# Performance work log

Measured on AMD Instinct MI355X. Metric: run time of the kernel, lower is better.

The kernel has to match this reference:

```python
import jax, jax.numpy as jnp
import numpy as np

D_MODEL = 1024
N_HEAD = 16
HEAD_DIM = D_MODEL // N_HEAD  # 64


def setup_inputs() -> dict:
    key = jax.random.key(0)
    ks = jax.random.split(key, 8)
    B, T, C = 4, 2048, D_MODEL
    s = 0.02
    return {
        "q": jax.random.normal(ks[0], (B, T, C), jnp.float32),
        "k": jax.random.normal(ks[1], (B, T, C), jnp.float32),
        "v": jax.random.normal(ks[2], (B, T, C), jnp.float32),
        "Wq": jax.random.normal(ks[3], (C, C), jnp.float32) * s,
        "Wk": jax.random.normal(ks[4], (C, HEAD_DIM), jnp.float32) * s,
        "Wv": jax.random.normal(ks[5], (C, HEAD_DIM), jnp.float32) * s,
        "Wp": jax.random.normal(ks[6], (C, C), jnp.float32) * s,
        "bp": jnp.zeros((C,), jnp.float32),
    }


def reference(q, k, v, Wq, Wk, Wv, Wp, bp):
    B, T, C = q.shape
    scale = 1.0 / jnp.sqrt(jnp.asarray(HEAD_DIM, q.dtype))
    # projections (torch Linear: x @ W.T, here weights stored as [in, out])
    q_proj = (q @ Wq).reshape(B, T, N_HEAD, HEAD_DIM)  # [B,T,H,D]
    k_proj = k @ Wk  # [B,T,D] single shared KV head
    v_proj = v @ Wv  # [B,T,D]
    # full O(T^2) scores per head, shared K
    wei = jnp.einsum("bqhd,bkd->bhqk", q_proj, k_proj) * scale  # [B,H,T,T]
    p = jax.nn.softmax(wei, axis=-1)
    out = jnp.einsum("bhqk,bkd->bqhd", p, v_proj).reshape(B, T, C)
    return out @ Wp + bp  # dropout p=0.0 -> identity
```

## Files before the change

### kernel.cpp

```cpp
#include <hip/hip_runtime.h>
#include <hip/hip_bf16.h>


#define B_ 4
#define T_ 2048
#define C_ 1024
#define H_ 16
#define D_ 64
#define BT_ (B_*T_)
#define CS_ 0.1803368801111204f

typedef short bfrag __attribute__((ext_vector_type(8)));
typedef float f32x4 __attribute__((ext_vector_type(4)));
typedef __bf16 bf2_t __attribute__((ext_vector_type(2)));

static __device__ inline short f2bf(float f){
    union { __bf16 h; short s; } c; c.h = (__bf16)f;
    return c.s;
}
static __device__ inline unsigned pk2(float a, float b){
    union { bf2_t v; unsigned u; } c;
    c.v[0] = (__bf16)a; c.v[1] = (__bf16)b;
    return c.u;
}

#if __has_builtin(__builtin_amdgcn_global_load_lds)
#define GLL16(g,l) __builtin_amdgcn_global_load_lds(                              \
    (const __attribute__((address_space(1))) void*)(g),                           \
    (__attribute__((address_space(3))) void*)(l), 16, 0, 0)
#else
#define GLL16(g,l) (*(uint4*)(l) = *(const uint4*)(g))
#endif

#if __has_builtin(__builtin_amdgcn_exp2f)
#define EXP2(x) __builtin_amdgcn_exp2f(x)
#else
#define EXP2(x) __expf((x)*0.693147180559945f)
#endif

__global__ __launch_bounds__(256) void prep_kernel(
    const float* __restrict__ q,
    const float* __restrict__ Wq, const float* __restrict__ Wk,
    const float* __restrict__ Wv, const float* __restrict__ Wp,
    short* __restrict__ qb16,
    short* __restrict__ WqT, short* __restrict__ WkT,
    short* __restrict__ WvT, short* __restrict__ WpT)
{
    int bx = blockIdx.x, tid = threadIdx.x;
    if (bx < 4096) {
        int i = (bx * 256 + tid) * 8;
        float4 a = *(const float4*)(q + i);
        float4 b = *(const float4*)(q + i + 4);
        uint4 o; o.x = pk2(a.x,a.y); o.y = pk2(a.z,a.w);
                 o.z = pk2(b.x,b.y); o.w = pk2(b.z,b.w);
        *(uint4*)(qb16 + i) = o;
        return;
    }
    __shared__ short Ls[64][65];
    int b2 = bx - 4096;
    const float* W; short* Wt; int N, idx;
    if (b2 < 256)      { W = Wq; Wt = WqT; N = 1024; idx = b2; }
    else if (b2 < 272) { W = Wk; Wt = WkT; N = 64;   idx = b2 - 256; }
    else if (b2 < 288) { W = Wv; Wt = WvT; N = 64;   idx = b2 - 272; }
    else               { W = Wp; Wt = WpT; N = 1024; idx = b2 - 288; }
    int nx = N >> 6;
    int n0 = (idx % nx) * 64, k0 = (idx / nx) * 64;
    {
        int kr = tid >> 2, c4 = (tid & 3) * 16;
        const float* g = W + (size_t)(k0 + kr) * N + n0 + c4;
        #pragma unroll
        for (int e = 0; e < 16; e++) Ls[kr][c4 + e] = f2bf(g[e]);
    }
    __syncthreads();
    {
        int nr = tid >> 2, kc = (tid & 3) * 16;
        __align__(16) short tmp[16];
        #pragma unroll
        for (int e = 0; e < 16; e++) tmp[e] = Ls[kc + e][nr];
        short* o = Wt + (size_t)(n0 + nr) * 1024 + k0 + kc;
        *(uint4*)(o)     = *(uint4*)tmp;
        *(uint4*)(o + 8) = *(uint4*)(tmp + 8);
    }
}

__global__ __launch_bounds__(256) void kvproj_kernel(
    const float* __restrict__ Ksrc, const float* __restrict__ Vsrc,
    const short* __restrict__ WkT, const short* __restrict__ WvT,
    short* __restrict__ Kfo, short* __restrict__ Vfo)
{
    __shared__ __align__(16) short As[2048];
    __shared__ __align__(16) short Bs[4096];
    int mode = blockIdx.x >> 8;
    int m0 = (blockIdx.x & 255) * 32;
    const float* A  = mode ? Vsrc : Ksrc;
    const short* Bt = mode ? WvT : WkT;
    short* Out      = mode ? Vfo : Kfo;

    int tid = threadIdx.x, w = tid >> 6, lane = tid & 63;
    int quad = lane >> 4, l16 = lane & 15;
    int wrow = (w >> 1) * 16, wcol = (w & 1) * 32;

    int arow = tid >> 3, acol = (tid & 7) * 8;
    int akh = acol >> 5, aoct = (acol >> 3) & 3;
    short* asl = As + ((((arow >> 4) * 2 + akh) * 64 + (arow & 15) * 4 + aoct) * 8);
    const float* ag = A + (size_t)(m0 + arow) * C_ + acol;
    int brow = tid >> 2, bcol = (tid & 3) * 16;
    int bkh = bcol >> 5, boct = (bcol >> 3) & 3;
    short* bsl = Bs + ((((brow >> 4) * 2 + bkh) * 64 + (brow & 15) * 4 + boct) * 8);
    const short* bg = Bt + (size_t)brow * C_ + bcol;

    f32x4 acc[2] = {};
    for (int k0 = 0; k0 < C_; k0 += 64) {
        __syncthreads();
        {
            float4 fa = *(const float4*)(ag + k0);
            float4 fb = *(const float4*)(ag + k0 + 4);
            uint4 pa; pa.x = pk2(fa.x,fa.y); pa.y = pk2(fa.z,fa.w);
                      pa.z = pk2(fb.x,fb.y); pa.w = pk2(fb.z,fb.w);
            *(uint4*)asl = pa;
            uint4 t0 = *(const uint4*)(bg + k0);
            uint4 t1 = *(const uint4*)(bg + k0 + 8);
            *(uint4*)bsl = t0; *(uint4*)(bsl + 8) = t1;
        }
        __syncthreads();
        #pragma unroll
        for (int ks = 0; ks < 2; ks++) {
            bfrag af = *(const bfrag*)(As + (((wrow >> 4) * 2 + ks) * 64 + l16 * 4 + quad) * 8);
            #pragma unroll
            for (int ni = 0; ni < 2; ni++) {
                int n = wcol + ni * 16;
                bfrag bf = *(const bfrag*)(Bs + (((n >> 4) * 2 + ks) * 64 + l16 * 4 + quad) * 8);
                acc[ni] = __builtin_amdgcn_mfma_f32_16x16x32_bf16(af, bf, acc[ni], 0, 0, 0);
            }
        }
    }
    if (mode == 0) {
        #pragma unroll
        for (int ni = 0; ni < 2; ni++)
            #pragma unroll
            for (int r = 0; r < 4; r++) {
                int key = m0 + wrow + quad * 4 + r;
                int d = wcol + ni * 16 + l16;
                size_t adr = (size_t)(key >> 6) * 4096 +
                    ((((d >> 5) * 4 + ((key >> 4) & 3)) * 4 + ((d >> 3) & 3)) * 16 + (key & 15)) * 8 + (d & 7);
                Out[adr] = f2bf(acc[ni][r]);
            }
    } else {
        #pragma unroll
        for (int ni = 0; ni < 2; ni++) {
            int ni2 = (w & 1) * 2 + ni;
            int key = m0 + wrow + quad * 4;
            int tile = key >> 6, kfk = (key >> 5) & 1, qv = (key >> 3) & 3;
            int jb = (quad & 1) * 4;
            uint2 pk; pk.x = pk2(acc[ni][0], acc[ni][1]); pk.y = pk2(acc[ni][2], acc[ni][3]);
            *(uint2*)(Out + (size_t)tile * 4096 + (((kfk * 4 + ni2) * 4 + qv) * 16 + l16) * 8 + jb) = pk;
        }
    }
}

__global__ __launch_bounds__(256, 4) void attn_fused_kernel(
    const short* __restrict__ qb16, const short* __restrict__ WqT,
    const short* __restrict__ Kfo,  const short* __restrict__ Vfo,
    short* __restrict__ Out)
{
    __shared__ __align__(16) short lds[8192];
    int qb = blockIdx.x, h = blockIdx.y, b = blockIdx.z;
    int tid = threadIdx.x, w = tid >> 6, lane = tid & 63;
    int quad = lane >> 4, l16 = lane & 15;
    short* As = lds;
    short* Bs = lds + 4096;
    short* Ps = lds + w * 2048;

    {
        int m0q = b * T_ + qb * 128;
        int cA2 = tid + 256;
        int rA1 = ((tid >> 6) << 4) + ((tid & 63) >> 2), oA1 = tid & 3;
        int rA2 = ((cA2 >> 6) << 4) + ((cA2 & 63) >> 2), oA2 = cA2 & 3;
        const short* gA1 = qb16 + (size_t)(m0q + rA1) * C_ + oA1 * 8;
        const short* gA2 = qb16 + (size_t)(m0q + rA2) * C_ + oA2 * 8;
        const short* gB  = WqT + (size_t)(h * 64 + rA1) * C_ + oA1 * 8;
        short* lA1 = As + tid * 8; short* lA2 = As + cA2 * 8;
        short* lB  = Bs + tid * 8;

        f32x4 qacc[2][4] = {};
        for (int k0 = 0; k0 < C_; k0 += 32) {
            __syncthreads();
            GLL16(gA1 + k0, lA1); GLL16(gA2 + k0, lA2); GLL16(gB + k0, lB);
            __syncthreads();
            bfrag af[2], bf[4];
            #pragma unroll
            for (int mi = 0; mi < 2; mi++)
                af[mi] = *(const bfrag*)(As + ((w * 2 + mi) * 64 + l16 * 4 + quad) * 8);
            #pragma unroll
            for (int ni = 0; ni < 4; ni++)
                bf[ni] = *(const bfrag*)(Bs + (ni * 64 + l16 * 4 + quad) * 8);
            #pragma unroll
            for (int mi = 0; mi < 2; mi++)
                #pragma unroll
                for (int ni = 0; ni < 4; ni++)
                    qacc[mi][ni] = __builtin_amdgcn_mfma_f32_16x16x32_bf16(af[mi], bf[ni], qacc[mi][ni], 0, 0, 0);
        }
        __syncthreads();
        #pragma unroll
        for (int mi = 0; mi < 2; mi++)
            #pragma unroll
            for (int ni = 0; ni < 4; ni++) {
                int base = ((ni >> 1) * 2 + mi) * 512 + ((ni & 1) * 2 + (l16 >> 3)) * 128 + (l16 & 7);
                #pragma unroll
                for (int r = 0; r < 4; r++)
                    Ps[base + (quad * 4 + r) * 8] = f2bf(qacc[mi][ni][r] * CS_);
            }
    }

    bfrag qf[2][2];
    #pragma unroll
    for (int nb = 0; nb < 2; nb++)
        #pragma unroll
        for (int kf = 0; kf < 2; kf++)
            qf[nb][kf] = *(const bfrag*)(Ps + (kf * 2 + nb) * 512 + quad * 128 + l16 * 8);

    const short* Kb = Kfo + (size_t)b * (T_ * D_);
    const short* Vb = Vfo + (size_t)b * (T_ * D_);
    int q0 = qb * 128 + w * 32;

    f32x4 o[4][2] = {};
    float lsum[2] = {0.f, 0.f};
    int fragoff = (quad * 16 + l16) * 8;

    for (int t = 0; t < T_ / 64; t++) {
        const short* Kt = Kb + t * 4096;
        const short* Vt = Vb + t * 4096;
        bfrag ka[2][4];
        #pragma unroll
        for (int kf = 0; kf < 2; kf++)
            #pragma unroll
            for (int mi = 0; mi < 4; mi++)
                ka[kf][mi] = *(const bfrag*)(Kt + (kf * 4 + mi) * 512 + fragoff);
        f32x4 s[4][2];
        #pragma unroll
        for (int mi = 0; mi < 4; mi++)
            #pragma unroll
            for (int nb = 0; nb < 2; nb++) {
                f32x4 z = {};
                z = __builtin_amdgcn_mfma_f32_16x16x32_bf16(ka[0][mi], qf[nb][0], z, 0, 0, 0);
                z = __builtin_amdgcn_mfma_f32_16x16x32_bf16(ka[1][mi], qf[nb][1], z, 0, 0, 0);
                s[mi][nb] = z;
            }
        bfrag va[2][4];
        #pragma unroll
        for (int kf = 0; kf < 2; kf++)
            #pragma unroll
            for (int mi = 0; mi < 4; mi++)
                va[kf][mi] = *(const bfrag*)(Vt + (kf * 4 + mi) * 512 + fragoff);
        #pragma unroll
        for (int nb = 0; nb < 2; nb++) {
            #pragma unroll
            for (int mi = 0; mi < 4; mi++) {
                float p0 = EXP2(s[mi][nb][0]);
                float p1 = EXP2(s[mi][nb][1]);
                float p2 = EXP2(s[mi][nb][2]);
                float p3 = EXP2(s[mi][nb][3]);
                lsum[nb] += (p0 + p1) + (p2 + p3);
                uint2 pk; pk.x = pk2(p0, p1); pk.y = pk2(p2, p3);
                int kf = mi >> 1, qp_ = (mi & 1) * 2 + (quad >> 1), jb = (quad & 1) * 4;
                *(uint2*)(Ps + (kf * 2 + nb) * 512 + qp_ * 128 + l16 * 8 + jb) = pk;
            }
        }
        #pragma unroll
        for (int nb = 0; nb < 2; nb++) {
            bfrag pf0 = *(const bfrag*)(Ps + (0 + nb) * 512 + quad * 128 + l16 * 8);
            bfrag pf1 = *(const bfrag*)(Ps + (2 + nb) * 512 + quad * 128 + l16 * 8);
            #pragma unroll
            for (int mi = 0; mi < 4; mi++) {
                o[mi][nb] = __builtin_amdgcn_mfma_f32_16x16x32_bf16(va[0][mi], pf0, o[mi][nb], 0, 0, 0);
                o[mi][nb] = __builtin_amdgcn_mfma_f32_16x16x32_bf16(va[1][mi], pf1, o[mi][nb], 0, 0, 0);
            }
        }
    }
    #pragma unroll
    for (int nb = 0; nb < 2; nb++) {
        float l = lsum[nb];
        l += __shfl_xor(l, 16, 64);
        l += __shfl_xor(l, 32, 64);
        float rl = 1.0f / l;
        size_t row = (size_t)(b * T_ + q0 + nb * 16 + l16);
        #pragma unroll
        for (int mi = 0; mi < 4; mi++) {
            uint2 pk; pk.x = pk2(o[mi][nb][0] * rl, o[mi][nb][1] * rl);
                      pk.y = pk2(o[mi][nb][2] * rl, o[mi][nb][3] * rl);
            *(uint2*)(Out + row * C_ + h * 64 + mi * 16 + quad * 4) = pk;
        }
    }
}

__global__ __launch_bounds__(256) void gemm_fin_kernel(
    const short* __restrict__ A, const short* __restrict__ Bt,
    const float* __restrict__ bias, float* __restrict__ Out)
{
    __shared__ __align__(16) short As[8192];
    __shared__ __align__(16) short Bs[8192];
    const int N = C_, K = C_;
    int tid = threadIdx.x, w = tid >> 6, lane = tid & 63;
    int quad = lane >> 4, l16 = lane & 15;
    int wm = (w >> 1) * 64, wn = (w & 1) * 64;
    int m0 = blockIdx.y * 128, n0 = blockIdx.x * 128;

    const short* gA[4]; short* lA[4];
    const short* gB[4]; short* lB[4];
    #pragma unroll
    for (int i = 0; i < 4; i++) {
        int c = tid + 256 * i;
        int row = ((c >> 7) << 4) + ((c & 63) >> 2);
        int koff = ((c >> 6) & 1) * 32 + (c & 3) * 8;
        gA[i] = A + (size_t)(m0 + row) * K + koff;
        lA[i] = As + c * 8;
        gB[i] = Bt + (size_t)(n0 + row) * K + koff;
        lB[i] = Bs + c * 8;
    }

    f32x4 acc[4][4] = {};
    for (int k0 = 0; k0 < K; k0 += 64) {
        __syncthreads();
        #pragma unroll
        for (int i = 0; i < 4; i++) GLL16(gA[i] + k0, lA[i]);
        #pragma unroll
        for (int i = 0; i < 4; i++) GLL16(gB[i] + k0, lB[i]);
        __syncthreads();
        #pragma unroll
        for (int ks = 0; ks < 2; ks++) {
            bfrag af[4], bf[4];
            #pragma unroll
            for (int i = 0; i < 4; i++)
                af[i] = *(const bfrag*)(As + ((((wm >> 4) + i) * 2 + ks) * 64 + l16 * 4 + quad) * 8);
            #pragma unroll
            for (int i = 0; i < 4; i++)
                bf[i] = *(const bfrag*)(Bs + ((((wn >> 4) + i) * 2 + ks) * 64 + l16 * 4 + quad) * 8);
            #pragma unroll
            for (int mi = 0; mi < 4; mi++)
                #pragma unroll
                for (int ni = 0; ni < 4; ni++)
                    acc[mi][ni] = __builtin_amdgcn_mfma_f32_16x16x32_bf16(af[mi], bf[ni], acc[mi][ni], 0, 0, 0);
        }
    }
    #pragma unroll
    for (int mi = 0; mi < 4; mi++)
        #pragma unroll
        for (int ni = 0; ni < 4; ni++) {
            int col = n0 + wn + ni * 16 + l16;
            float bv = bias[col];
            #pragma unroll
            for (int r = 0; r < 4; r++) {
                int row = m0 + wm + mi * 16 + quad * 4 + r;
                Out[(size_t)row * N + col] = acc[mi][ni][r] + bv;
            }
        }
}

extern "C" void kernel_launch(void* const* d_in, const int* in_sizes, int n_in,
                              void* d_out, int out_size, void* d_ws, size_t ws_size,
                              hipStream_t stream) {
    const float* q  = (const float*)d_in[0];
    const float* k  = (const float*)d_in[1];
    const float* v  = (const float*)d_in[2];
    const float* Wq = (const float*)d_in[3];
    const float* Wk = (const float*)d_in[4];
    const float* Wv = (const float*)d_in[5];
    const float* Wp = (const float*)d_in[6];
    const float* bp = (const float*)d_in[7];
    float* out = (float*)d_out;

    char* ws = (char*)d_ws;
    short* qb16     = (short*)(ws);
    short* attn_out = (short*)(ws + (16u << 20));
    short* WqT  = (short*)(ws + (32u << 20));
    short* WpT  = (short*)(ws + (34u << 20));
    short* Kfo  = (short*)(ws + (36u << 20));
    short* Vfo  = (short*)(ws + (37u << 20));
    short* WkT  = (short*)(ws + (38u << 20));
    short* WvT  = (short*)(ws + (38u << 20) + (1u << 18));

    dim3 blk(256);
    prep_kernel<<<4640, blk, 0, stream>>>(q, Wq, Wk, Wv, Wp, qb16, WqT, WkT, WvT, WpT);
    kvproj_kernel<<<512, blk, 0, stream>>>(k, v, WkT, WvT, Kfo, Vfo);
    attn_fused_kernel<<<dim3(16, 16, 4), blk, 0, stream>>>(qb16, WqT, Kfo, Vfo, attn_out);
    gemm_fin_kernel<<<dim3(8, 64), blk, 0, stream>>>(attn_out, WpT, bp, out);
}
```

Before: 287.9 us.

## Split Q projection into standalone GEMM that converts fp32 q on load

Takes the Q projection out of the attention kernel and runs it as a separate 128x128-tile bf16 MFMA GEMM. That GEMM reads fp32 q directly, converts it to bf16 while staging into LDS, and writes a pre-scaled bf16 Q buffer. The separate fp32-to-bf16 conversion pass in the prep kernel is removed, and the attention kernel now loads its Q fragments straight from global memory. This cuts the per-block 64-wide projection work and its many barriers out of attention, at the cost of an extra kernel launch and a global round trip for Q.

```diff
diff --git a/kernel.cpp b/kernel.cpp
--- a/kernel.cpp
+++ b/kernel.cpp
@@ -39,25 +39,13 @@
 #endif
 
 __global__ __launch_bounds__(256) void prep_kernel(
-    const float* __restrict__ q,
     const float* __restrict__ Wq, const float* __restrict__ Wk,
     const float* __restrict__ Wv, const float* __restrict__ Wp,
-    short* __restrict__ qb16,
     short* __restrict__ WqT, short* __restrict__ WkT,
     short* __restrict__ WvT, short* __restrict__ WpT)
 {
-    int bx = blockIdx.x, tid = threadIdx.x;
-    if (bx < 4096) {
-        int i = (bx * 256 + tid) * 8;
-        float4 a = *(const float4*)(q + i);
-        float4 b = *(const float4*)(q + i + 4);
-        uint4 o; o.x = pk2(a.x,a.y); o.y = pk2(a.z,a.w);
-                 o.z = pk2(b.x,b.y); o.w = pk2(b.z,b.w);
-        *(uint4*)(qb16 + i) = o;
-        return;
-    }
+    int b2 = blockIdx.x, tid = threadIdx.x;
     __shared__ short Ls[64][65];
-    int b2 = bx - 4096;
     const float* W; short* Wt; int N, idx;
     if (b2 < 256)      { W = Wq; Wt = WqT; N = 1024; idx = b2; }
     else if (b2 < 272) { W = Wk; Wt = WkT; N = 64;   idx = b2 - 256; }
@@ -81,6 +69,79 @@
         *(uint4*)(o)     = *(uint4*)tmp;
         *(uint4*)(o + 8) = *(uint4*)(tmp + 8);
     }
+}
+
+__global__ __launch_bounds__(256) void qproj_kernel(
+    const float* __restrict__ Aq, const short* __restrict__ Bt,
+    short* __restrict__ Qp)
+{
+    __shared__ __align__(16) short As[8192];
+    __shared__ __align__(16) short Bs[8192];
+    const int K = C_;
+    int tid = threadIdx.x, w = tid >> 6, lane = tid & 63;
+    int quad = lane >> 4, l16 = lane & 15;
+    int wm = (w >> 1) * 64, wn = (w & 1) * 64;
+    int m0 = blockIdx.y * 128, n0 = blockIdx.x * 128;
+
+    const float* gA[8]; short* lA[8];
+    #pragma unroll
+    for (int i = 0; i < 8; i++) {
+        int c = tid + 256 * i;
+        int row = c >> 4, fc = c & 15;
+        gA[i] = Aq + (size_t)(m0 + row) * K + fc * 4;
+        int m16 = row >> 4, l16r = row & 15;
+        int ks = fc >> 3, q4 = (fc >> 1) & 3, e0 = (fc & 1) * 4;
+        lA[i] = As + ((m16 * 2 + ks) * 64 + l16r * 4 + q4) * 8 + e0;
+    }
+    const short* gB[4]; short* lB[4];
+    #pragma unroll
+    for (int i = 0; i < 4; i++) {
+        int c = tid + 256 * i;
+        int row = ((c >> 7) << 4) + ((c & 63) >> 2);
+        int koff = ((c >> 6) & 1) * 32 + (c & 3) * 8;
+        gB[i] = Bt + (size_t)(n0 + row) * K + koff;
+        lB[i] = Bs + c * 8;
+    }
+
+    f32x4 acc[4][4] = {};
+    for (int k0 = 0; k0 < K; k0 += 64) {
+        __syncthreads();
+        #pragma unroll
+        for (int i = 0; i < 8; i++) {
+            float4 f = *(const float4*)(gA[i] + k0);
+            uint2 p; p.x = pk2(f.x, f.y); p.y = pk2(f.z, f.w);
+            *(uint2*)lA[i] = p;
+        }
+        #pragma unroll
+        for (int i = 0; i < 4; i++) GLL16(gB[i] + k0, lB[i]);
+        __syncthreads();
+        #pragma unroll
+        for (int ks = 0; ks < 2; ks++) {
+            bfrag af[4], bf[4];
+            #pragma unroll
+            for (int i = 0; i < 4; i++)
+                af[i] = *(const bfrag*)(As + ((((wm >> 4) + i) * 2 + ks) * 64 + l16 * 4 + quad) * 8);
+            #pragma unroll
+            for (int i = 0; i < 4; i++)
+                bf[i] = *(const bfrag*)(Bs + ((((wn >> 4) + i) * 2 + ks) * 64 + l16 * 4 + quad) * 8);
+            #pragma unroll
+            for (int mi = 0; mi < 4; mi++)
+                #pragma unroll
+                for (int ni = 0; ni < 4; ni++)
+                    acc[mi][ni] = __builtin_amdgcn_mfma_f32_16x16x32_bf16(af[mi], bf[ni], acc[mi][ni], 0, 0, 0);
+        }
+    }
+    #pragma unroll
+    for (int mi = 0; mi < 4; mi++)
+        #pragma unroll
+        for (int ni = 0; ni < 4; ni++) {
+            int col = n0 + wn + ni * 16 + l16;
+            #pragma unroll
+            for (int r = 0; r < 4; r++) {
+                int row = m0 + wm + mi * 16 + quad * 4 + r;
+                Qp[(size_t)row * C_ + col] = f2bf(acc[mi][ni][r] * CS_);
+            }
+        }
 }
 
 __global__ __launch_bounds__(256) void kvproj_kernel(
@@ -158,66 +219,24 @@
     }
 }
 
-__global__ __launch_bounds__(256, 4) void attn_fused_kernel(
-    const short* __restrict__ qb16, const short* __restrict__ WqT,
-    const short* __restrict__ Kfo,  const short* __restrict__ Vfo,
-    short* __restrict__ Out)
+__global__ __launch_bounds__(256, 4) void attn_kernel(
+    const short* __restrict__ Qp, const short* __restrict__ Kfo,
+    const short* __restrict__ Vfo, short* __restrict__ Out)
 {
     __shared__ __align__(16) short lds[8192];
     int qb = blockIdx.x, h = blockIdx.y, b = blockIdx.z;
     int tid = threadIdx.x, w = tid >> 6, lane = tid & 63;
     int quad = lane >> 4, l16 = lane & 15;
-    short* As = lds;
-    short* Bs = lds + 4096;
     short* Ps = lds + w * 2048;
-
-    {
-        int m0q = b * T_ + qb * 128;
-        int cA2 = tid + 256;
-        int rA1 = ((tid >> 6) << 4) + ((tid & 63) >> 2), oA1 = tid & 3;
-        int rA2 = ((cA2 >> 6) << 4) + ((cA2 & 63) >> 2), oA2 = cA2 & 3;
-        const short* gA1 = qb16 + (size_t)(m0q + rA1) * C_ + oA1 * 8;
-        const short* gA2 = qb16 + (size_t)(m0q + rA2) * C_ + oA2 * 8;
-        const short* gB  = WqT + (size_t)(h * 64 + rA1) * C_ + oA1 * 8;
-        short* lA1 = As + tid * 8; short* lA2 = As + cA2 * 8;
-        short* lB  = Bs + tid * 8;
-
-        f32x4 qacc[2][4] = {};
-        for (int k0 = 0; k0 < C_; k0 += 32) {
-            __syncthreads();
-            GLL16(gA1 + k0, lA1); GLL16(gA2 + k0, lA2); GLL16(gB + k0, lB);
-            __syncthreads();
-            bfrag af[2], bf[4];
-            #pragma unroll
-            for (int mi = 0; mi < 2; mi++)
-                af[mi] = *(const bfrag*)(As + ((w * 2 + mi) * 64 + l16 * 4 + quad) * 8);
-            #pragma unroll
-            for (int ni = 0; ni < 4; ni++)
-                bf[ni] = *(const bfrag*)(Bs + (ni * 64 + l16 * 4 + quad) * 8);
-            #pragma unroll
-            for (int mi = 0; mi < 2; mi++)
-                #pragma unroll
-                for (int ni = 0; ni < 4; ni++)
-                    qacc[mi][ni] = __builtin_amdgcn_mfma_f32_16x16x32_bf16(af[mi], bf[ni], qacc[mi][ni], 0, 0, 0);
-        }
-        __syncthreads();
-        #pragma unroll
-        for (int mi = 0; mi < 2; mi++)
-            #pragma unroll
-            for (int ni = 0; ni < 4; ni++) {
-                int base = ((ni >> 1) * 2 + mi) * 512 + ((ni & 1) * 2 + (l16 >> 3)) * 128 + (l16 & 7);
-                #pragma unroll
-                for (int r = 0; r < 4; r++)
-                    Ps[base + (quad * 4 + r) * 8] = f2bf(qacc[mi][ni][r] * CS_);
-            }
-    }
+    int m0q = b * T_ + qb * 128;
 
     bfrag qf[2][2];
     #pragma unroll
     for (int nb = 0; nb < 2; nb++)
         #pragma unroll
         for (int kf = 0; kf < 2; kf++)
-            qf[nb][kf] = *(const bfrag*)(Ps + (kf * 2 + nb) * 512 + quad * 128 + l16 * 8);
+            qf[nb][kf] = *(const bfrag*)(Qp +
+                (size_t)(m0q + w * 32 + nb * 16 + l16) * C_ + h * 64 + kf * 32 + quad * 8);
 
     const short* Kb = Kfo + (size_t)b * (T_ * D_);
     const short* Vb = Vfo + (size_t)b * (T_ * D_);
@@ -370,7 +389,7 @@
     float* out = (float*)d_out;
 
     char* ws = (char*)d_ws;
-    short* qb16     = (short*)(ws);
+    short* Qp       = (short*)(ws);
     short* attn_out = (short*)(ws + (16u << 20));
     short* WqT  = (short*)(ws + (32u << 20));
     short* WpT  = (short*)(ws + (34u << 20));
@@ -380,8 +399,9 @@
     short* WvT  = (short*)(ws + (38u << 20) + (1u << 18));
 
     dim3 blk(256);
-    prep_kernel<<<4640, blk, 0, stream>>>(q, Wq, Wk, Wv, Wp, qb16, WqT, WkT, WvT, WpT);
+    prep_kernel<<<544, blk, 0, stream>>>(Wq, Wk, Wv, Wp, WqT, WkT, WvT, WpT);
+    qproj_kernel<<<dim3(8, 64), blk, 0, stream>>>(q, WqT, Qp);
     kvproj_kernel<<<512, blk, 0, stream>>>(k, v, WkT, WvT, Kfo, Vfo);
-    attn_fused_kernel<<<dim3(16, 16, 4), blk, 0, stream>>>(qb16, WqT, Kfo, Vfo, attn_out);
+    attn_kernel<<<dim3(16, 16, 4), blk, 0, stream>>>(Qp, Kfo, Vfo, attn_out);
     gemm_fin_kernel<<<dim3(8, 64), blk, 0, stream>>>(attn_out, WpT, bp, out);
 }
```

Result: slower. 299.7 us (+4.1%).
